# Kernel optimization log

Hardware: AMD Instinct MI355X
Metric: run time of the kernel (lower is better)

## Reference

```python
import jax, jax.numpy as jnp
import numpy as np

B_GRAPHS = 16
N_PER_GRAPH = 128
N_NODES = B_GRAPHS * N_PER_GRAPH  # 2048
HIDDEN = 256
N_HEADS = 8
HEAD_DIM = HIDDEN // N_HEADS
N_LAYERS = 4
K_RPE = 4
N_EDGES = 32768
NUM_NODE_FEATS = 32
NUM_EDGE_TYPES = 16
MAX_DEGREE = 100
MLP_HID = HIDDEN // 2


def _layernorm(x, s, b):
    m = x.mean(-1, keepdims=True)
    v = jnp.var(x, axis=-1, keepdims=True)
    return (x - m) / jnp.sqrt(v + 1e-5) * s + b


def setup_inputs() -> dict:
    key = jax.random.key(0)
    ks = jax.random.split(key, 24)
    s = 0.02
    x_idx = jax.random.randint(ks[0], (N_NODES,), 0, NUM_NODE_FEATS)
    # edges are intra-graph (the torch code drops cross-graph edges)
    src = jax.random.randint(ks[1], (N_EDGES,), 0, N_NODES)
    dst = (src // N_PER_GRAPH) * N_PER_GRAPH + jax.random.randint(ks[2], (N_EDGES,), 0, N_PER_GRAPH)
    edge_index = jnp.stack([src, dst])
    edge_attr = jax.random.randint(ks[3], (N_EDGES,), 0, NUM_EDGE_TYPES)
    batch = jnp.repeat(jnp.arange(B_GRAPHS), N_PER_GRAPH)
    L = N_LAYERS
    return {
        'x_idx': x_idx, 'edge_index': edge_index, 'edge_attr': edge_attr, 'batch': batch,
        'node_emb': jax.random.normal(ks[4], (NUM_NODE_FEATS, HIDDEN)) * s,
        'edge_emb': jax.random.normal(ks[5], (NUM_EDGE_TYPES, N_HEADS)) * s,
        'degree_emb': jax.random.normal(ks[6], (MAX_DEGREE + 1, HIDDEN)) * s,
        'rpe_W1': jax.random.normal(ks[7], (K_RPE + 1, MLP_HID)) * s,
        'rpe_b1': jnp.zeros((MLP_HID,)),
        'rpe_W2': jax.random.normal(ks[8], (MLP_HID, N_HEADS)) * s,
        'rpe_b2': jnp.zeros((N_HEADS,)),
        'Wq': jax.random.normal(ks[9], (L, HIDDEN, HIDDEN)) * s, 'bq': jnp.zeros((L, HIDDEN)),
        'Wk': jax.random.normal(ks[10], (L, HIDDEN, HIDDEN)) * s, 'bk': jnp.zeros((L, HIDDEN)),
        'Wv': jax.random.normal(ks[11], (L, HIDDEN, HIDDEN)) * s, 'bv': jnp.zeros((L, HIDDEN)),
        'Wo': jax.random.normal(ks[12], (L, HIDDEN, HIDDEN)) * s, 'bo': jnp.zeros((L, HIDDEN)),
        'ln1_s': jnp.ones((L, HIDDEN)), 'ln1_b': jnp.zeros((L, HIDDEN)),
        'ln2_s': jnp.ones((L, HIDDEN)), 'ln2_b': jnp.zeros((L, HIDDEN)),
        'ff_W1': jax.random.normal(ks[13], (L, HIDDEN, 2 * HIDDEN)) * s, 'ff_b1': jnp.zeros((L, 2 * HIDDEN)),
        'ff_W2': jax.random.normal(ks[14], (L, 2 * HIDDEN, HIDDEN)) * s, 'ff_b2': jnp.zeros((L, HIDDEN)),
    }


def _forward(x_idx, edge_index, edge_attr, batch,
             node_emb, edge_emb, degree_emb, rpe_W1, rpe_b1, rpe_W2, rpe_b2,
             Wq, bq, Wk, bk, Wv, bv, Wo, bo, ln1_s, ln1_b, ln2_s, ln2_b,
             ff_W1, ff_b1, ff_W2, ff_b2):
    B, n, H, N = B_GRAPHS, N_PER_GRAPH, N_HEADS, N_NODES
    x = node_emb[x_idx]                               # [N, d]
    src, dst = edge_index[0], edge_index[1]
    # degrees from source endpoints (scatter_add in torch)
    deg = jnp.zeros((N,), jnp.int32).at[src].add(1)
    deg_c = jnp.minimum(deg, MAX_DEGREE)

    # ---- RRWP + edge-type attention bias, block-diagonal over graphs ----
    g = batch[src]
    intra = (batch[src] == batch[dst])                # torch code skips cross-graph edges
    u = src % n
    v = dst % n
    intra_f = intra.astype(jnp.float32)
    inv_du = intra_f / jnp.maximum(deg[src], 1).astype(jnp.float32)
    inv_dv = intra_f / jnp.maximum(deg[dst], 1).astype(jnp.float32)
    # random-walk transition matrix per graph [B, n, n]
    T = (jnp.zeros((B, n, n), jnp.float32)
         .at[g, u, v].add(inv_du)
         .at[g, v, u].add(inv_dv))
    # symmetric edge-type bias per graph [B, n, n, H]
    ev = edge_emb[edge_attr] * intra_f[:, None]
    EB = (jnp.zeros((B, n, n, H), jnp.float32)
          .at[g, u, v].add(ev)
          .at[g, v, u].add(ev))
    # walk powers I, T, T^2, ..., T^K -> [B, n, n, K+1]
    I = jnp.broadcast_to(jnp.eye(n, dtype=jnp.float32), (B, n, n))
    powers = [I, T]
    cur = T
    for _ in range(2, K_RPE + 1):
        cur = cur @ T
        powers.append(cur)
    walk = jnp.stack(powers, axis=-1)
    pair = jax.nn.relu(walk @ rpe_W1 + rpe_b1) @ rpe_W2 + rpe_b2   # [B, n, n, H]
    block = (pair + EB).transpose(0, 3, 1, 2)                      # [B, H, n, n]
    ib = jnp.arange(B)
    full = jnp.full((H, B, n, B, n), -jnp.inf, jnp.float32)
    full = full.at[:, ib, :, ib, :].set(block)                     # diag blocks
    attn_bias = full.reshape(H, N, N)

    # ---- transformer stack ----
    deg_vec = degree_emb[deg_c]
    scale = 1.0 / jnp.sqrt(jnp.float32(HEAD_DIM))
    for l in range(N_LAYERS):
        x = x + deg_vec
        Q = (x @ Wq[l] + bq[l]).reshape(N, H, HEAD_DIM)
        K_ = (x @ Wk[l] + bk[l]).reshape(N, H, HEAD_DIM)
        V = (x @ Wv[l] + bv[l]).reshape(N, H, HEAD_DIM)
        scores = jnp.einsum('ihd,jhd->hij', Q, K_) * scale + attn_bias
        aw = jax.nn.softmax(scores, axis=-1)
        out = jnp.einsum('hij,jhd->ihd', aw, V).reshape(N, HIDDEN)
        out = out @ Wo[l] + bo[l]
        x = _layernorm(x + out, ln1_s[l], ln1_b[l])
        ff = jax.nn.relu(x @ ff_W1[l] + ff_b1[l]) @ ff_W2[l] + ff_b2[l]
        x = _layernorm(x + ff, ln2_s[l], ln2_b[l])
    # global add pool
    return jax.ops.segment_sum(x, batch, num_segments=B)


def reference(x_idx, edge_index, edge_attr, batch,
              node_emb, edge_emb, degree_emb, rpe_W1, rpe_b1, rpe_W2, rpe_b2,
              Wq, bq, Wk, bk, Wv, bv, Wo, bo, ln1_s, ln1_b, ln2_s, ln2_b,
              ff_W1, ff_b1, ff_W2, ff_b2):
    return _forward(x_idx, edge_index, edge_attr, batch,
                    node_emb, edge_emb, degree_emb, rpe_W1, rpe_b1, rpe_W2, rpe_b2,
                    Wq, bq, Wk, bk, Wv, bv, Wo, bo, ln1_s, ln1_b, ln2_s, ln2_b,
                    ff_W1, ff_b1, ff_W2, ff_b2)
```

## Files before the change

kernel.cpp:

```cpp
#include <hip/hip_runtime.h>
#include <hip/hip_bf16.h>

#define B_GRAPHS 16
#define NPG 128
#define NN 2048
#define HIDDEN 256
#define N_HEADS 8
#define HEAD_DIM 32
#define N_LAYERS 4
#define N_EDGES 32768
#define MLP_HID 128
#define MAX_DEG 100

typedef __hip_bfloat16 bf16;
typedef unsigned short ushort_t;
typedef __attribute__((ext_vector_type(8))) short short8;
typedef __attribute__((ext_vector_type(4))) float f32x4;

__device__ __forceinline__ float us2f(ushort_t u) {
    return __uint_as_float(((unsigned)u) << 16);
}
__device__ __forceinline__ ushort_t f2us(float f) {
    unsigned u = __float_as_uint(f);
    return (ushort_t)((u + 0x7FFFu + ((u >> 16) & 1u)) >> 16);
}
__device__ __forceinline__ bool is_bf16_mode(const unsigned* probe) {
    return probe[0] != 0x3F800000u;
}
#define MFMA16(a, b, c) __builtin_amdgcn_mfma_f32_16x16x32_bf16(a, b, c, 0, 0, 0)

__device__ __forceinline__ void gload_lds16(const void* g, void* l) {
    __builtin_amdgcn_global_load_lds(
        (const __attribute__((address_space(1))) unsigned int*)g,
        (__attribute__((address_space(3))) unsigned int*)l, 16, 0, 0);
}
#define SBAR __builtin_amdgcn_s_barrier()
#define WAITPIPE asm volatile("s_waitcnt vmcnt(16) lgkmcnt(0)" ::: "memory")
#define WAITLAST asm volatile("s_waitcnt vmcnt(0) lgkmcnt(0)" ::: "memory")
#define LBAR do { asm volatile("s_waitcnt lgkmcnt(0)" ::: "memory"); SBAR; \
                  asm volatile("" ::: "memory"); } while (0)

#define NW 23
__device__ const int c_wsizes[NW] = {
    8192, 128, 25856, 640, 128, 1024, 8,
    262144, 1024, 262144, 1024, 262144, 1024, 262144, 1024,
    1024, 1024, 1024, 1024,
    524288, 2048, 524288, 1024};
#define TOTW 2144392

#define OFF_NODE_EMB 0
#define OFF_EDGE_EMB 8192
#define OFF_DEG_EMB  8320
#define OFF_RPE_W1   34176
#define OFF_RPE_B1   34816
#define OFF_RPE_W2   34944
#define OFF_RPE_B2   35968
#define OFF_BO       1087624
#define OFF_LN1S     1088648
#define OFF_LN1B     1089672
#define OFF_LN2S     1090696
#define OFF_LN2B     1091720
#define OFF_FFB1     1617032
#define OFF_FFB2     2143368

#define WB_QKV 0
#define WB_O   786432
#define WB_F1  1048576
#define WB_F2  1572864
#define WB_TOT 2097152
#define QKVB_TOT 3072

struct SrcPtrs { const void* p[NW]; };

__global__ void convert_kernel(SrcPtrs sp, const unsigned* __restrict__ probe,
                               float* __restrict__ Wc, float* __restrict__ qkvb) {
    int i = blockIdx.x * 256 + threadIdx.x;
    bool isbf = is_bf16_mode(probe);
    auto rd = [&](int seg, int off) -> float {
        return isbf ? us2f(((const ushort_t*)sp.p[seg])[off])
                    : ((const float*)sp.p[seg])[off];
    };
    if (i < TOTW) {
        int seg = 0, off = i;
        while (seg < NW - 1 && off >= c_wsizes[seg]) { off -= c_wsizes[seg]; seg++; }
        Wc[i] = rd(seg, off);
    } else if (i < TOTW + QKVB_TOT) {
        int j = i - TOTW;
        int l = j / 768, n = j % 768, which = n >> 8, nn = n & 255;
        int seg = (which == 0) ? 8 : (which == 1) ? 10 : 12;
        qkvb[j] = rd(seg, l * 256 + nn);
    }
}

__global__ __launch_bounds__(256) void transpose_pack(SrcPtrs sp,
                                                      const unsigned* __restrict__ probe,
                                                      ushort_t* __restrict__ WB) {
    __shared__ float tile[32][33];
    int b = blockIdx.x;
    bool isbf = is_bf16_mode(probe);
    int seg, soff, srcN, k0, n0, dK;
    size_t doff;
    if (b < 768) {
        int mat = b >> 6, t = b & 63;
        int l = mat / 3, which = mat % 3;
        seg = 7 + which * 2;
        soff = l * 65536; srcN = 256;
        k0 = (t >> 3) * 32; n0 = (t & 7) * 32;
        doff = (size_t)l * 196608 + (size_t)which * 65536; dK = 256;
    } else if (b < 1024) {
        int u = b - 768, l = u >> 6, t = u & 63;
        seg = 13; soff = l * 65536; srcN = 256;
        k0 = (t >> 3) * 32; n0 = (t & 7) * 32;
        doff = WB_O + (size_t)l * 65536; dK = 256;
    } else if (b < 1536) {
        int u = b - 1024, l = u >> 7, t = u & 127;
        seg = 19; soff = l * 131072; srcN = 512;
        k0 = (t >> 4) * 32; n0 = (t & 15) * 32;
        doff = WB_F1 + (size_t)l * 131072; dK = 256;
    } else {
        int u = b - 1536, l = u >> 7, t = u & 127;
        seg = 21; soff = l * 131072; srcN = 256;
        k0 = (t >> 3) * 32; n0 = (t & 7) * 32;
        doff = WB_F2 + (size_t)l * 131072; dK = 512;
    }
    int xcol = threadIdx.x & 31, y8 = threadIdx.x >> 5;
    const void* srcp = sp.p[seg];
#pragma unroll
    for (int rr = 0; rr < 4; rr++) {
        int row = y8 * 4 + rr;
        int off = soff + (k0 + row) * srcN + n0 + xcol;
        tile[row][xcol] = isbf ? us2f(((const ushort_t*)srcp)[off])
                               : ((const float*)srcp)[off];
    }
    __syncthreads();
#pragma unroll
    for (int rr = 0; rr < 4; rr++) {
        int nrow = y8 * 4 + rr;
        WB[doff + (size_t)(n0 + nrow) * dK + k0 + xcol] = f2us(tile[xcol][nrow]);
    }
}

__global__ void zero_kernel(f32x4* __restrict__ p) {
    f32x4 z;
    z[0] = 0.f; z[1] = 0.f; z[2] = 0.f; z[3] = 0.f;
    p[blockIdx.x * 256 + threadIdx.x] = z;
}

__global__ void deg_kernel(const int* __restrict__ src, int* __restrict__ deg) {
    int e = blockIdx.x * blockDim.x + threadIdx.x;
    if (e < N_EDGES) atomicAdd(&deg[src[e]], 1);
}

__global__ void gather_xadd(const int* __restrict__ xidx, const int* __restrict__ deg,
                            const float* __restrict__ emb, const float* __restrict__ demb,
                            float* __restrict__ x, ushort_t* __restrict__ xb) {
    int i = blockIdx.x * blockDim.x + threadIdx.x;
    int node = i >> 8, c = i & 255;
    float v = emb[xidx[node] * HIDDEN + c] + demb[min(deg[node], MAX_DEG) * HIDDEN + c];
    x[i] = v;
    xb[i] = f2us(v);
}

__global__ void scatter_kernel(const int* __restrict__ ei, const int* __restrict__ eattr,
                               const int* __restrict__ batch, const int* __restrict__ deg,
                               const float* __restrict__ edge_emb,
                               float* __restrict__ T, float* __restrict__ bias) {
    int idx = blockIdx.x * blockDim.x + threadIdx.x;
    int e = idx >> 3, h = idx & 7;
    int s = ei[e], d = ei[N_EDGES + e];
    if (batch[s] != batch[d]) return;
    int g = batch[s];
    int u = s & (NPG - 1), v = d & (NPG - 1);
    if (h == 0) {
        atomicAdd(&T[(g * NPG + u) * NPG + v], 1.0f / (float)max(deg[s], 1));
        atomicAdd(&T[(g * NPG + v) * NPG + u], 1.0f / (float)max(deg[d], 1));
    }
    float ev = edge_emb[eattr[e] * N_HEADS + h];
    atomicAdd(&bias[(((size_t)(g * N_HEADS + h) * NPG + u) * NPG + v)], ev);
    atomicAdd(&bias[(((size_t)(g * N_HEADS + h) * NPG + v) * NPG + u)], ev);
}

__global__ void matmul128(const float* __restrict__ A, const float* __restrict__ B,
                          float* __restrict__ C) {
    int g = blockIdx.x / NPG;
    int row = blockIdx.x % NPG;
    int col = threadIdx.x;
    const float* Ag = A + (size_t)g * NPG * NPG;
    const float* Bg = B + (size_t)g * NPG * NPG;
    __shared__ float arow[NPG];
    arow[col] = Ag[row * NPG + col];
    __syncthreads();
    float acc = 0.f;
#pragma unroll 8
    for (int k = 0; k < NPG; k++) acc += arow[k] * Bg[k * NPG + col];
    C[((size_t)g * NPG + row) * NPG + col] = acc;
}

__global__ void matmul128_dual(const float* __restrict__ T2, const float* __restrict__ T,
                               float* __restrict__ T3, float* __restrict__ T4) {
    int half = blockIdx.x >> 11;
    int bid = blockIdx.x & 2047;
    int g = bid / NPG, row = bid % NPG, col = threadIdx.x;
    const float* Ag = T2 + (size_t)g * NPG * NPG;
    const float* Bg = (half ? T2 : T) + (size_t)g * NPG * NPG;
    float* Cg = (half ? T4 : T3) + (size_t)g * NPG * NPG;
    __shared__ float arow[NPG];
    arow[col] = Ag[row * NPG + col];
    __syncthreads();
    float acc = 0.f;
#pragma unroll 8
    for (int k = 0; k < NPG; k++) acc += arow[k] * Bg[k * NPG + col];
    Cg[row * NPG + col] = acc;
}

__global__ __launch_bounds__(256) void rpe_kernel(
    const float* __restrict__ T, const float* __restrict__ T2,
    const float* __restrict__ T3, const float* __restrict__ T4,
    const float* __restrict__ W1, const float* __restrict__ b1,
    const float* __restrict__ W2, const float* __restrict__ b2,
    float* __restrict__ bias) {
    __shared__ float sW1[5][MLP_HID];
    __shared__ float sb1[MLP_HID];
    __shared__ float sW2[MLP_HID][N_HEADS];
    int t = threadIdx.x;
    for (int i = t; i < 5 * MLP_HID; i += 256) sW1[i / MLP_HID][i % MLP_HID] = W1[i];
    for (int i = t; i < MLP_HID; i += 256) sb1[i] = b1[i];
    for (int i = t; i < MLP_HID * N_HEADS; i += 256) sW2[i / N_HEADS][i % N_HEADS] = W2[i];
    __syncthreads();
    int p = blockIdx.x * 256 + t;
    int g = p / (NPG * NPG);
    int rem = p % (NPG * NPG);
    int i = rem / NPG, j = rem % NPG;
    float f0 = (i == j) ? 1.f : 0.f;
    float f1 = T[p], f2 = T2[p], f3 = T3[p], f4 = T4[p];
    float acc[N_HEADS];
#pragma unroll
    for (int h = 0; h < N_HEADS; h++) acc[h] = b2[h];
#pragma unroll 4
    for (int m = 0; m < MLP_HID; m++) {
        float hv = sb1[m] + f0 * sW1[0][m] + f1 * sW1[1][m] + f2 * sW1[2][m] +
                   f3 * sW1[3][m] + f4 * sW1[4][m];
        hv = fmaxf(hv, 0.f);
#pragma unroll
        for (int h = 0; h < N_HEADS; h++) acc[h] += hv * sW2[m][h];
    }
#pragma unroll
    for (int h = 0; h < N_HEADS; h++)
        bias[(((size_t)(g * N_HEADS + h) * NPG + i) * NPG + j)] += acc[h];
}

__global__ __launch_bounds__(256, 1) void qkv_attn(
    const ushort_t* __restrict__ x_bf, const ushort_t* __restrict__ WT,
    const float* __restrict__ qb, const float* __restrict__ bias,
    ushort_t* __restrict__ ao) {
    int bid = blockIdx.x;
    int g = bid >> 4, h = (bid >> 1) & 7, half = bid & 1;
    int wave = threadIdx.x >> 6, lane = threadIdx.x & 63;
    int lr = lane & 15, lq = lane >> 4;

    __shared__ ushort_t Qs[64][40];
    __shared__ ushort_t Ks[NPG][40];
    __shared__ ushort_t VT[32][136];
    __shared__ ushort_t P[4][16][136];

    const ushort_t* xg = x_bf + (size_t)g * NPG * HIDDEN;
    int qrow = half * 64 + wave * 16;
    int kvrow = wave * 32;

    short8 Aq[8], Akv[2][8], Bq[2][8], Bk[2][8], Bv[2][8];
#pragma unroll
    for (int kk = 0; kk < 8; kk++) {
        Aq[kk] = *(const short8*)(xg + (size_t)(qrow + lr) * 256 + kk * 32 + lq * 8);
#pragma unroll
        for (int i = 0; i < 2; i++)
            Akv[i][kk] = *(const short8*)(xg + (size_t)(kvrow + i * 16 + lr) * 256 +
                                          kk * 32 + lq * 8);
#pragma unroll
        for (int j = 0; j < 2; j++) {
            int n = h * 32 + j * 16 + lr;
            Bq[j][kk] = *(const short8*)(WT + (size_t)n * 256 + kk * 32 + lq * 8);
            Bk[j][kk] = *(const short8*)(WT + (size_t)(n + 256) * 256 + kk * 32 + lq * 8);
            Bv[j][kk] = *(const short8*)(WT + (size_t)(n + 512) * 256 + kk * 32 + lq * 8);
        }
    }
    float bqv[2], bkv[2], bvv[2];
#pragma unroll
    for (int j = 0; j < 2; j++) {
        int c = h * 32 + j * 16 + lr;
        bqv[j] = qb[c]; bkv[j] = qb[256 + c]; bvv[j] = qb[512 + c];
    }

    f32x4 qa[2]{}, ka[2][2]{}, va[2][2]{};
#pragma unroll
    for (int kk = 0; kk < 8; kk++)
#pragma unroll
        for (int j = 0; j < 2; j++) {
            qa[j] = MFMA16(Aq[kk], Bq[j][kk], qa[j]);
#pragma unroll
            for (int i = 0; i < 2; i++) {
                ka[i][j] = MFMA16(Akv[i][kk], Bk[j][kk], ka[i][j]);
                va[i][j] = MFMA16(Akv[i][kk], Bv[j][kk], va[i][j]);
            }
        }

    const float* bg = bias + (size_t)(g * N_HEADS + h) * NPG * NPG;
    float bgv[8][4];
#pragma unroll
    for (int r = 0; r < 4; r++) {
        int i = half * 64 + wave * 16 + lq * 4 + r;
#pragma unroll
        for (int jt = 0; jt < 8; jt++)
            bgv[jt][r] = bg[(size_t)i * NPG + jt * 16 + lr];
    }

#pragma unroll
    for (int j = 0; j < 2; j++) {
        int c = j * 16 + lr;
#pragma unroll
        for (int r = 0; r < 4; r++) {
            Qs[wave * 16 + lq * 4 + r][c] = f2us(qa[j][r] + bqv[j]);
#pragma unroll
            for (int i = 0; i < 2; i++) {
                int row = kvrow + i * 16 + lq * 4 + r;
                Ks[row][c] = f2us(ka[i][j][r] + bkv[j]);
                VT[c][row] = f2us(va[i][j][r] + bvv[j]);
            }
        }
    }
    __syncthreads();

    short8 qf = *(const short8*)(&Qs[wave * 16 + lr][lq * 8]);
    f32x4 S[8];
    f32x4 zero;
    zero[0] = 0.f; zero[1] = 0.f; zero[2] = 0.f; zero[3] = 0.f;
#pragma unroll
    for (int jt = 0; jt < 8; jt++) {
        short8 kf = *(const short8*)(&Ks[jt * 16 + lr][lq * 8]);
        S[jt] = MFMA16(qf, kf, zero);
    }

    const float scale = 0.17677669529663687f;
    float lrow[4];
#pragma unroll
    for (int r = 0; r < 4; r++) {
        float mx = -1e30f;
#pragma unroll
        for (int jt = 0; jt < 8; jt++) {
            float s = S[jt][r] * scale + bgv[jt][r];
            S[jt][r] = s;
            mx = fmaxf(mx, s);
        }
#pragma unroll
        for (int m = 1; m < 16; m <<= 1) mx = fmaxf(mx, __shfl_xor(mx, m));
        float sum = 0.f;
#pragma unroll
        for (int jt = 0; jt < 8; jt++) {
            float e = __expf(S[jt][r] - mx);
            S[jt][r] = e;
            sum += e;
        }
#pragma unroll
        for (int m = 1; m < 16; m <<= 1) sum += __shfl_xor(sum, m);
        lrow[r] = sum;
    }

#pragma unroll
    for (int jt = 0; jt < 8; jt++)
#pragma unroll
        for (int r = 0; r < 4; r++)
            P[wave][lq * 4 + r][jt * 16 + lr] = f2us(S[jt][r]);

    f32x4 O[2]{};
#pragma unroll
    for (int k0 = 0; k0 < NPG; k0 += 32) {
        short8 pa = *(const short8*)(&P[wave][lr][k0 + lq * 8]);
#pragma unroll
        for (int dt = 0; dt < 2; dt++) {
            short8 vb = *(const short8*)(&VT[dt * 16 + lr][k0 + lq * 8]);
            O[dt] = MFMA16(pa, vb, O[dt]);
        }
    }
#pragma unroll
    for (int r = 0; r < 4; r++) {
        float inv = 1.f / lrow[r];
        int row = g * NPG + half * 64 + wave * 16 + lq * 4 + r;
#pragma unroll
        for (int dt = 0; dt < 2; dt++)
            ao[(size_t)row * HIDDEN + h * 32 + dt * 16 + lr] = f2us(O[dt][r] * inv);
    }
}

__global__ __launch_bounds__(256, 1) void fused_mlp(
    const ushort_t* __restrict__ ao, const ushort_t* __restrict__ WoT,
    const float* __restrict__ bo, const float* __restrict__ ln1s,
    const float* __restrict__ ln1b,
    const ushort_t* __restrict__ F1T, const ushort_t* __restrict__ F2T,
    const float* __restrict__ fb1, const float* __restrict__ fb2,
    const float* __restrict__ ln2s, const float* __restrict__ ln2b,
    const float* __restrict__ xin, const int* __restrict__ deg,
    const float* __restrict__ demb, int add_deg,
    float* __restrict__ xout, ushort_t* __restrict__ xb) {
    int m0 = blockIdx.x * 8;
    int wave = threadIdx.x >> 6, lane = threadIdx.x & 63;
    int lr = lane & 15, lq = lane >> 4;
    int ar = m0 + (lr & 7);

    __shared__ ushort_t Wbuf[2][32768];
    __shared__ ushort_t xs_bf[8][264];
    __shared__ ushort_t ffh[8][520];
    __shared__ float ws[4][16], qs[4][16];

    auto stageO = [&](int h, int b) {
        const char* gW = (const char*)WoT;
        char* lb = (char*)&Wbuf[b][0] + wave * 16384;
#pragma unroll
        for (int it = 0; it < 16; it++) {
            int j = wave * 16384 + it * 1024 + lane * 16;
            int n = j >> 8, off = j & 255;
            gload_lds16(gW + n * 512 + h * 256 + (off ^ ((n & 7) << 4)), lb + it * 1024);
        }
        __builtin_amdgcn_sched_barrier(0);
    };
    auto stageF1 = [&](int q, int b) {
        const char* gW = (const char*)F1T;
        char* lb = (char*)&Wbuf[b][0] + wave * 16384;
#pragma unroll
        for (int it = 0; it < 16; it++) {
            int j = wave * 16384 + it * 1024 + lane * 16;
            int n = j >> 9, off = j & 511;
            gload_lds16(gW + (q * 128 + n) * 512 + (off ^ ((n & 7) << 4)), lb + it * 1024);
        }
        __builtin_amdgcn_sched_barrier(0);
    };
    auto stageF2 = [&](int q, int b) {
        const char* gW = (const char*)F2T;
        char* lb = (char*)&Wbuf[b][0] + wave * 16384;
#pragma unroll
        for (int it = 0; it < 16; it++) {
            int j = wave * 16384 + it * 1024 + lane * 16;
            int n = j >> 8, off = j & 255;
            gload_lds16(gW + n * 1024 + q * 256 + (off ^ ((n & 7) << 4)), lb + it * 1024);
        }
        __builtin_amdgcn_sched_barrier(0);
    };

    float bo_v[4], l1s[4], l1b[4], fb2v[4], l2s[4], l2b[4], xres[4][4], fb1q[4][2];
#pragma unroll
    for (int jt = 0; jt < 4; jt++) {
        int col = wave * 64 + jt * 16 + lr;
        bo_v[jt] = bo[col]; l1s[jt] = ln1s[col]; l1b[jt] = ln1b[col];
        fb2v[jt] = fb2[col]; l2s[jt] = ln2s[col]; l2b[jt] = ln2b[col];
#pragma unroll
        for (int r = 0; r < 4; r++) {
            int row = m0 + ((lq * 4 + r) & 7);
            xres[jt][r] = xin[(size_t)row * 256 + col];
        }
    }
#pragma unroll
    for (int q = 0; q < 4; q++)
#pragma unroll
        for (int t = 0; t < 2; t++)
            fb1q[q][t] = fb1[q * 128 + wave * 32 + t * 16 + lr];
    int dg4[4];
    if (add_deg) {
#pragma unroll
        for (int r = 0; r < 4; r++)
            dg4[r] = min(deg[m0 + ((lq * 4 + r) & 7)], MAX_DEG);
    }
    short8 Af[8];
#pragma unroll
    for (int t = 0; t < 8; t++)
        Af[t] = *(const short8*)(ao + (size_t)ar * 256 + t * 32 + lq * 8);

    stageO(0, 0);
    stageO(1, 1);

    f32x4 acc[4]{};
#pragma unroll
    for (int h = 0; h < 2; h++) {
        WAITPIPE; SBAR; asm volatile("" ::: "memory");
#pragma unroll
        for (int kk = 0; kk < 4; kk++) {
            short8 a = Af[h * 4 + kk];
#pragma unroll
            for (int jt = 0; jt < 4; jt++) {
                int n = wave * 64 + jt * 16 + lr;
                int bo_ = n * 256 + ((kk * 64 + lq * 16) ^ ((n & 7) << 4));
                short8 bf = *(const short8*)((const char*)&Wbuf[h][0] + bo_);
                acc[jt] = MFMA16(a, bf, acc[jt]);
            }
        }
        LBAR;
        if (h == 0) stageF1(0, 0);
        else        stageF1(1, 1);
    }

    float valLN[4][4], meanst[4];
#pragma unroll
    for (int r = 0; r < 4; r++) {
        float s = 0.f;
#pragma unroll
        for (int jt = 0; jt < 4; jt++) {
            float v = acc[jt][r] + bo_v[jt] + xres[jt][r];
            valLN[jt][r] = v;
            s += v;
        }
#pragma unroll
        for (int m = 1; m < 16; m <<= 1) s += __shfl_xor(s, m);
        if (lr == 0) ws[wave][lq * 4 + r] = s;
    }
    LBAR;
#pragma unroll
    for (int r = 0; r < 4; r++) {
        int rr = lq * 4 + r;
        float mean = (ws[0][rr] + ws[1][rr] + ws[2][rr] + ws[3][rr]) * (1.f / 256.f);
        meanst[r] = mean;
        float q = 0.f;
#pragma unroll
        for (int jt = 0; jt < 4; jt++) {
            float d = valLN[jt][r] - mean;
            q += d * d;
        }
#pragma unroll
        for (int m = 1; m < 16; m <<= 1) q += __shfl_xor(q, m);
        if (lr == 0) qs[wave][rr] = q;
    }
    LBAR;
#pragma unroll
    for (int r = 0; r < 4; r++) {
        int rr = lq * 4 + r;
        float var = (qs[0][rr] + qs[1][rr] + qs[2][rr] + qs[3][rr]) * (1.f / 256.f);
        float rstd = rsqrtf(var + 1e-5f);
#pragma unroll
        for (int jt = 0; jt < 4; jt++) {
            int col = wave * 64 + jt * 16 + lr;
            float y = (valLN[jt][r] - meanst[r]) * rstd * l1s[jt] + l1b[jt];
            valLN[jt][r] = y;
            if (rr < 8) xs_bf[rr][col] = f2us(y);
        }
    }

#pragma unroll
    for (int q = 0; q < 4; q++) {
        WAITPIPE; SBAR; asm volatile("" ::: "memory");
        f32x4 a1[2]{};
#pragma unroll
        for (int kk = 0; kk < 8; kk++) {
            short8 a = *(const short8*)(&xs_bf[lr & 7][kk * 32 + lq * 8]);
#pragma unroll
            for (int t = 0; t < 2; t++) {
                int n = wave * 32 + t * 16 + lr;
                int bo_ = n * 512 + ((kk * 64 + lq * 16) ^ ((n & 7) << 4));
                short8 bf = *(const short8*)((const char*)&Wbuf[q & 1][0] + bo_);
                a1[t] = MFMA16(a, bf, a1[t]);
            }
        }
#pragma unroll
        for (int t = 0; t < 2; t++) {
            int col = q * 128 + wave * 32 + t * 16 + lr;
#pragma unroll
            for (int r = 0; r < 4; r++) {
                int rr = lq * 4 + r;
                if (rr < 8) ffh[rr][col] = f2us(fmaxf(a1[t][r] + fb1q[q][t], 0.f));
            }
        }
        LBAR;
        if (q < 2) stageF1(q + 2, q & 1);
        else       stageF2(q - 2, q & 1);
    }

    f32x4 acc2[4]{};
#pragma unroll
    for (int q = 0; q < 4; q++) {
        if (q == 3) { WAITLAST; } else { WAITPIPE; }
        SBAR; asm volatile("" ::: "memory");
#pragma unroll
        for (int kk = 0; kk < 4; kk++) {
            short8 a = *(const short8*)(&ffh[lr & 7][q * 128 + kk * 32 + lq * 8]);
#pragma unroll
            for (int jt = 0; jt < 4; jt++) {
                int n = wave * 64 + jt * 16 + lr;
                int bo_ = n * 256 + ((kk * 64 + lq * 16) ^ ((n & 7) << 4));
                short8 bf = *(const short8*)((const char*)&Wbuf[q & 1][0] + bo_);
                acc2[jt] = MFMA16(a, bf, acc2[jt]);
            }
        }
        LBAR;
        if (q < 2) stageF2(q + 2, q & 1);
    }

    float val2[4][4];
#pragma unroll
    for (int r = 0; r < 4; r++) {
        int rr = lq * 4 + r;
        float s = 0.f;
#pragma unroll
        for (int jt = 0; jt < 4; jt++) {
            float v = acc2[jt][r] + fb2v[jt] + valLN[jt][r];
            val2[jt][r] = v;
            s += v;
        }
#pragma unroll
        for (int m = 1; m < 16; m <<= 1) s += __shfl_xor(s, m);
        if (lr == 0) ws[wave][rr] = s;
    }
    __syncthreads();
#pragma unroll
    for (int r = 0; r < 4; r++) {
        int rr = lq * 4 + r;
        float mean = (ws[0][rr] + ws[1][rr] + ws[2][rr] + ws[3][rr]) * (1.f / 256.f);
        meanst[r] = mean;
        float q = 0.f;
#pragma unroll
        for (int jt = 0; jt < 4; jt++) {
            float d = val2[jt][r] - mean;
            q += d * d;
        }
#pragma unroll
        for (int m = 1; m < 16; m <<= 1) q += __shfl_xor(q, m);
        if (lr == 0) qs[wave][rr] = q;
    }
    __syncthreads();
#pragma unroll
    for (int r = 0; r < 4; r++) {
        int rr = lq * 4 + r;
        float var = (qs[0][rr] + qs[1][rr] + qs[2][rr] + qs[3][rr]) * (1.f / 256.f);
        float rstd = rsqrtf(var + 1e-5f);
        if (rr < 8) {
            int row = m0 + rr;
#pragma unroll
            for (int jt = 0; jt < 4; jt++) {
                int col = wave * 64 + jt * 16 + lr;
                float y = (val2[jt][r] - meanst[r]) * rstd * l2s[jt] + l2b[jt];
                if (add_deg) y += demb[dg4[r] * 256 + col];
                xout[(size_t)row * 256 + col] = y;
                xb[(size_t)row * 256 + col] = f2us(y);
            }
        }
    }
}

__global__ void pool_kernel(const float* __restrict__ x, void* __restrict__ out,
                            const unsigned* __restrict__ probe) {
    int b = blockIdx.x;
    int c = threadIdx.x;
    float acc = 0.f;
#pragma unroll 4
    for (int i = 0; i < NPG; i++) acc += x[(size_t)(b * NPG + i) * HIDDEN + c];
    if (is_bf16_mode(probe))
        ((bf16*)out)[b * HIDDEN + c] = __float2bfloat16(acc);
    else
        ((float*)out)[b * HIDDEN + c] = acc;
}

extern "C" void kernel_launch(void* const* d_in, const int* in_sizes, int n_in,
                              void* d_out, int out_size, void* d_ws, size_t ws_size,
                              hipStream_t stream) {
    const int* x_idx      = (const int*)d_in[0];
    const int* edge_index = (const int*)d_in[1];
    const int* edge_attr  = (const int*)d_in[2];
    const int* batch      = (const int*)d_in[3];
    const unsigned* probe = (const unsigned*)d_in[19];

    char* base = (char*)d_ws;
    float* Wc    = (float*)base;       base += (size_t)TOTW * 4;
    float* x     = (float*)base;       base += (size_t)NN * HIDDEN * 4;
    float* T     = (float*)base;       base += 262144 * 4;
    float* bias  = (float*)base;       base += (size_t)2097152 * 4;
    int*   deg   = (int*)base;         base += 2048 * 4;
    float* T2    = (float*)base;       base += 262144 * 4;
    float* T3    = (float*)base;       base += 262144 * 4;
    float* T4    = (float*)base;       base += 262144 * 4;
    float* qkvb  = (float*)base;       base += QKVB_TOT * 4;
    ushort_t* WB    = (ushort_t*)base; base += (size_t)WB_TOT * 2;
    ushort_t* x_bf  = (ushort_t*)base; base += (size_t)NN * HIDDEN * 2;
    ushort_t* ao_bf = (ushort_t*)base; base += (size_t)NN * HIDDEN * 2;

    SrcPtrs sp;
    for (int i = 0; i < NW; i++) sp.p[i] = d_in[4 + i];

    zero_kernel<<<2306, 256, 0, stream>>>((f32x4*)T);
    convert_kernel<<<(TOTW + QKVB_TOT + 255) / 256, 256, 0, stream>>>(sp, probe, Wc, qkvb);
    transpose_pack<<<2048, 256, 0, stream>>>(sp, probe, WB);
    deg_kernel<<<N_EDGES / 256, 256, 0, stream>>>(edge_index, deg);
    gather_xadd<<<NN, 256, 0, stream>>>(x_idx, deg, Wc + OFF_NODE_EMB, Wc + OFF_DEG_EMB,
                                        x, x_bf);
    scatter_kernel<<<N_EDGES * 8 / 256, 256, 0, stream>>>(edge_index, edge_attr, batch, deg,
                                                          Wc + OFF_EDGE_EMB, T, bias);
    matmul128<<<B_GRAPHS * NPG, NPG, 0, stream>>>(T, T, T2);
    matmul128_dual<<<2 * B_GRAPHS * NPG, NPG, 0, stream>>>(T2, T, T3, T4);
    rpe_kernel<<<(B_GRAPHS * NPG * NPG) / 256, 256, 0, stream>>>(
        T, T2, T3, T4, Wc + OFF_RPE_W1, Wc + OFF_RPE_B1, Wc + OFF_RPE_W2, Wc + OFF_RPE_B2,
        bias);

    for (int l = 0; l < N_LAYERS; l++) {
        qkv_attn<<<2 * B_GRAPHS * N_HEADS, 256, 0, stream>>>(
            x_bf, WB + WB_QKV + (size_t)l * 196608, qkvb + l * 768, bias, ao_bf);
        fused_mlp<<<NN / 8, 256, 0, stream>>>(
            ao_bf, WB + WB_O + (size_t)l * 65536, Wc + OFF_BO + l * 256,
            Wc + OFF_LN1S + l * 256, Wc + OFF_LN1B + l * 256,
            WB + WB_F1 + (size_t)l * 131072, WB + WB_F2 + (size_t)l * 131072,
            Wc + OFF_FFB1 + l * 512, Wc + OFF_FFB2 + l * 256,
            Wc + OFF_LN2S + l * 256, Wc + OFF_LN2B + l * 256, x,
            deg, Wc + OFF_DEG_EMB, (l < N_LAYERS - 1) ? 1 : 0, x, x_bf);
    }
    pool_kernel<<<B_GRAPHS, 256, 0, stream>>>(x, d_out, probe);
}
```

Measured before the change: 356.8 us.

## Stage QKV weight slices through LDS with async global-to-LDS loads

Replaces the per-wave register loads of the Q/K/V weight slices with cooperative asynchronous global-to-LDS copies using a swizzled layout. The three slices are issued as separate stages so the Q, K and V MFMA loops can start as each stage lands, overlapping with the attention-bias loads. The goal is to remove redundant per-wave global weight traffic and register pressure. In exchange it adds 48KB of LDS, hand-counted vmcnt waits and barriers that depend on the exact number of outstanding loads.

Measured after the change: 343.4 us. 3.8% less time.

```diff
diff --git a/kernel.cpp b/kernel.cpp
--- a/kernel.cpp
+++ b/kernel.cpp
@@ -258,6 +258,7 @@
     int wave = threadIdx.x >> 6, lane = threadIdx.x & 63;
     int lr = lane & 15, lq = lane >> 4;
 
+    __shared__ char Wbuf[3][16384];
     __shared__ ushort_t Qs[64][40];
     __shared__ ushort_t Ks[NPG][40];
     __shared__ ushort_t VT[32][136];
@@ -267,7 +268,7 @@
     int qrow = half * 64 + wave * 16;
     int kvrow = wave * 32;
 
-    short8 Aq[8], Akv[2][8], Bq[2][8], Bk[2][8], Bv[2][8];
+    short8 Aq[8], Akv[2][8];
 #pragma unroll
     for (int kk = 0; kk < 8; kk++) {
         Aq[kk] = *(const short8*)(xg + (size_t)(qrow + lr) * 256 + kk * 32 + lq * 8);
@@ -275,13 +276,6 @@
         for (int i = 0; i < 2; i++)
             Akv[i][kk] = *(const short8*)(xg + (size_t)(kvrow + i * 16 + lr) * 256 +
                                           kk * 32 + lq * 8);
-#pragma unroll
-        for (int j = 0; j < 2; j++) {
-            int n = h * 32 + j * 16 + lr;
-            Bq[j][kk] = *(const short8*)(WT + (size_t)n * 256 + kk * 32 + lq * 8);
-            Bk[j][kk] = *(const short8*)(WT + (size_t)(n + 256) * 256 + kk * 32 + lq * 8);
-            Bv[j][kk] = *(const short8*)(WT + (size_t)(n + 512) * 256 + kk * 32 + lq * 8);
-        }
     }
     float bqv[2], bkv[2], bvv[2];
 #pragma unroll
@@ -289,19 +283,23 @@
         int c = h * 32 + j * 16 + lr;
         bqv[j] = qb[c]; bkv[j] = qb[256 + c]; bvv[j] = qb[512 + c];
     }
-
-    f32x4 qa[2]{}, ka[2][2]{}, va[2][2]{};
-#pragma unroll
-    for (int kk = 0; kk < 8; kk++)
-#pragma unroll
-        for (int j = 0; j < 2; j++) {
-            qa[j] = MFMA16(Aq[kk], Bq[j][kk], qa[j]);
-#pragma unroll
-            for (int i = 0; i < 2; i++) {
-                ka[i][j] = MFMA16(Akv[i][kk], Bk[j][kk], ka[i][j]);
-                va[i][j] = MFMA16(Akv[i][kk], Bv[j][kk], va[i][j]);
-            }
-        }
+    asm volatile("s_waitcnt vmcnt(0) lgkmcnt(0)" ::: "memory");
+
+    auto stageW = [&](int rowbase, int c) {
+        const char* gW = (const char*)WT;
+        char* lb = &Wbuf[c][0] + wave * 4096;
+#pragma unroll
+        for (int it = 0; it < 4; it++) {
+            int j = wave * 4096 + it * 1024 + lane * 16;
+            int n = j >> 9, off = j & 511;
+            gload_lds16(gW + (size_t)(rowbase + n) * 512 + (off ^ ((n & 7) << 4)),
+                        lb + it * 1024);
+        }
+        __builtin_amdgcn_sched_barrier(0);
+    };
+    stageW(h * 32, 0);
+    stageW(256 + h * 32, 1);
+    stageW(512 + h * 32, 2);
 
     const float* bg = bias + (size_t)(g * N_HEADS + h) * NPG * NPG;
     float bgv[8][4];
@@ -312,6 +310,39 @@
         for (int jt = 0; jt < 8; jt++)
             bgv[jt][r] = bg[(size_t)i * NPG + jt * 16 + lr];
     }
+    __builtin_amdgcn_sched_barrier(0);
+
+    auto rdW = [&](int c, int jt, int kk) -> short8 {
+        int n = jt * 16 + lr;
+        int off = n * 512 + ((kk * 64 + lq * 16) ^ ((n & 7) << 4));
+        return *(const short8*)(&Wbuf[c][off]);
+    };
+
+    f32x4 qa[2]{}, ka[2][2]{}, va[2][2]{};
+    asm volatile("s_waitcnt vmcnt(40)" ::: "memory"); SBAR;
+#pragma unroll
+    for (int kk = 0; kk < 8; kk++)
+#pragma unroll
+        for (int j = 0; j < 2; j++)
+            qa[j] = MFMA16(Aq[kk], rdW(0, j, kk), qa[j]);
+
+    asm volatile("s_waitcnt vmcnt(36)" ::: "memory"); SBAR;
+#pragma unroll
+    for (int kk = 0; kk < 8; kk++)
+#pragma unroll
+        for (int j = 0; j < 2; j++)
+#pragma unroll
+            for (int i = 0; i < 2; i++)
+                ka[i][j] = MFMA16(Akv[i][kk], rdW(1, j, kk), ka[i][j]);
+
+    asm volatile("s_waitcnt vmcnt(32)" ::: "memory"); SBAR;
+#pragma unroll
+    for (int kk = 0; kk < 8; kk++)
+#pragma unroll
+        for (int j = 0; j < 2; j++)
+#pragma unroll
+            for (int i = 0; i < 2; i++)
+                va[i][j] = MFMA16(Akv[i][kk], rdW(2, j, kk), va[i][j]);
 
 #pragma unroll
     for (int j = 0; j < 2; j++) {
```
